# Optimization experiments

Measured on AMD Instinct MI355X. Metric: run time of the kernel, lower is better.

Reference implementation:

```python
import jax, jax.numpy as jnp
import numpy as np

SIGMA = 0.3
EPS = 1e-8  # torch CosineSimilarity eps


def _normal_log_prob(x, sigma=SIGMA):
    # torch.distributions.Normal(1, sigma).log_prob(x)
    return -0.5 * ((x - 1.0) / sigma) ** 2 - jnp.log(sigma) - 0.5 * jnp.log(2.0 * jnp.pi)


def _entropy_term(lp):
    # -(exp(lp) * lp).sum()
    return -jnp.sum(jnp.exp(lp) * lp)


def setup_inputs() -> dict:
    key = jax.random.key(0)
    kx, ky = jax.random.split(key)
    ex = jax.random.normal(kx, (8192, 512), dtype=jnp.float32)
    ey = jax.random.normal(ky, (8192, 512), dtype=jnp.float32)
    return {"ex": ex, "ey": ey}


def reference(ex, ey):
    # cosine similarity matrix C[n, m] = <ex_n, ey_m> / (||ex_n|| * ||ey_m||)
    xn = ex / jnp.maximum(jnp.linalg.norm(ex, axis=-1, keepdims=True), EPS)
    yn = ey / jnp.maximum(jnp.linalg.norm(ey, axis=-1, keepdims=True), EPS)
    C = jnp.einsum('nd,md->nm', xn, yn)  # [N, M]
    # condense_side == 'both'
    lp_right = _normal_log_prob(jnp.max(C, axis=-1))  # [N]
    lp_left = _normal_log_prob(jnp.max(C, axis=0))    # [M]
    return (_entropy_term(lp_right), _entropy_term(lp_left))
```

## Files before the change

### kernel.cpp

```cpp
#include <hip/hip_runtime.h>
#include <hip/hip_bf16.h>
#include <stdint.h>

#define NROWS 8192
#define DIM   512
#define NP    4
#define NSTEP 4
#define NTILE 4
#define FSCALE 16.0f
#define INV_FS2 (1.0f / 256.0f)
#define SCALE1 0x7F7F7F7F

typedef unsigned char u8;
typedef float f32x4 __attribute__((ext_vector_type(4)));
typedef int i32x4 __attribute__((ext_vector_type(4)));
typedef int i32x8 __attribute__((ext_vector_type(8)));

__device__ __forceinline__ unsigned fenc(float f) {
  unsigned u = __float_as_uint(f);
  return (u & 0x80000000u) ? ~u : (u | 0x80000000u);
}
__device__ __forceinline__ float fdec(unsigned u) {
  unsigned b = (u & 0x80000000u) ? (u ^ 0x80000000u) : ~u;
  return __uint_as_float(b);
}

#if __has_builtin(__builtin_amdgcn_cvt_pk_fp8_f32)
#define HAVE_CVT_PK_FP8 1
#else
__device__ __forceinline__ u8 f2e4m3(float f) {
  unsigned u = __float_as_uint(f);
  unsigned sgn = (u >> 24) & 0x80u;
  unsigned au = u & 0x7FFFFFFFu;
  if (au < 0x3C800000u) return (u8)sgn;
  unsigned r = au + 0x7FFFFu + ((au >> 20) & 1u);
  int e = (int)((r >> 23) & 0xFF) - 127;
  unsigned m = (r >> 20) & 7u;
  if (e > 8) return (u8)(sgn | 0x7Eu);
  return (u8)(sgn | ((unsigned)(e + 7) << 3) | m);
}
#endif

__device__ __forceinline__ void async16(const void* g, void* l) {
  __builtin_amdgcn_global_load_lds(
      (const __attribute__((address_space(1))) unsigned int*)g,
      (__attribute__((address_space(3))) unsigned int*)l, 16, 0, 0);
}

__global__ __launch_bounds__(512) void normf_kernel(
    const float* __restrict__ ex, const float* __restrict__ ey,
    u8* __restrict__ Xf, u8* __restrict__ Yf,
    unsigned* __restrict__ enc_init) {
  const int pb = blockIdx.x;
  const int p = pb & 511;
  const float* src = (pb < 512) ? ex : ey;
  u8* dst = (pb < 512) ? Xf : Yf;
  const int t = threadIdx.x, lane = t & 63, w = t >> 6;
  const int fr = lane & 15, hi = lane >> 4;
  if (pb < 32) {
    enc_init[pb * 512 + t] = fenc(-512.0f);
  }
  __shared__ float part[16][8];
  float e[2][8];
  float ss = 0.f;
#pragma unroll
  for (int c = 0; c < 2; ++c) {
    const int q = w + c * 8;
    const float* g = src + (size_t)(p * 16 + fr) * DIM + q * 32 + hi * 8;
    float4 v0 = *(const float4*)g;
    float4 v1 = *(const float4*)(g + 4);
    e[c][0] = v0.x; e[c][1] = v0.y; e[c][2] = v0.z; e[c][3] = v0.w;
    e[c][4] = v1.x; e[c][5] = v1.y; e[c][6] = v1.z; e[c][7] = v1.w;
#pragma unroll
    for (int j = 0; j < 8; ++j) ss += e[c][j] * e[c][j];
  }
  ss += __shfl_xor(ss, 16);
  ss += __shfl_xor(ss, 32);
  if (lane < 16) part[lane][w] = ss;
  __syncthreads();
  float tot = 0.f;
#pragma unroll
  for (int i = 0; i < 8; ++i) tot += part[fr][i];
  const float sc = FSCALE / fmaxf(sqrtf(tot), 1e-8f);
#pragma unroll
  for (int c = 0; c < 2; ++c) {
    const int q = w + c * 8;
#if HAVE_CVT_PK_FP8
    int lo = 0, hi2 = 0;
    lo = __builtin_amdgcn_cvt_pk_fp8_f32(e[c][0] * sc, e[c][1] * sc, lo, false);
    lo = __builtin_amdgcn_cvt_pk_fp8_f32(e[c][2] * sc, e[c][3] * sc, lo, true);
    hi2 = __builtin_amdgcn_cvt_pk_fp8_f32(e[c][4] * sc, e[c][5] * sc, hi2, false);
    hi2 = __builtin_amdgcn_cvt_pk_fp8_f32(e[c][6] * sc, e[c][7] * sc, hi2, true);
    const unsigned long long pk =
        (unsigned long long)(unsigned)lo | ((unsigned long long)(unsigned)hi2 << 32);
#else
    unsigned long long pk = 0;
#pragma unroll
    for (int j = 0; j < 8; ++j)
      pk |= (unsigned long long)f2e4m3(e[c][j] * sc) << (8 * j);
#endif
    const int f = q >> 2;
    const int kg = q & 3;
    const int olane = fr + kg * 16;
    const int half = hi >> 1;
    const size_t addr = (size_t)(p * NP + f) * 2048 + half * 1024 +
                        olane * 16 + (hi & 1) * 8;
    *(unsigned long long*)(dst + addr) = pk;
  }
}

__global__ __launch_bounds__(256, 3) void gemm_max_kernel(
    const u8* __restrict__ Xf, const u8* __restrict__ Yf,
    unsigned* __restrict__ rowmax, unsigned* __restrict__ colmax) {
  __shared__ u8 lds[16][2048];

  const int t = threadIdx.x, lane = t & 63, w = t >> 6;
  const int wr = w >> 1, wc = w & 1;

  const int raw = blockIdx.x, xcd = raw & 7, l = raw >> 3;
  const int brow = (l & 63) * 128;
  const int bcol0 = (xcd * 2 + (l >> 6)) * 512;
  const int browP = brow >> 4;

  f32x4 acc[4][4];
#pragma unroll
  for (int m = 0; m < 4; ++m)
#pragma unroll
    for (int n = 0; n < 4; ++n) acc[m][n] = (f32x4){0.f, 0.f, 0.f, 0.f};

  const u8* gA0 = Xf + (size_t)(browP + 2 * w) * (NP * 2048) + lane * 16;
  const u8* gA1 = Xf + (size_t)(browP + 2 * w + 1) * (NP * 2048) + lane * 16;
  const u8* gBb = Yf + (size_t)(bcol0 >> 4) * (NP * 2048) + lane * 16;

#pragma unroll 1
  for (int u = 0; u < NTILE * NSTEP; ++u) {
    const int h = u & 3;
    const int tileP = (u >> 2) * 8;
    const size_t o = (size_t)h * 2048;
    __syncthreads();
    {
      const u8* gB0 = gBb + (size_t)(tileP + 2 * w) * (NP * 2048);
      const u8* gB1 = gBb + (size_t)(tileP + 2 * w + 1) * (NP * 2048);
#pragma unroll
      for (int half = 0; half < 2; ++half) {
        async16(gA0 + o + half * 1024, &lds[2 * w][half * 1024]);
        async16(gA1 + o + half * 1024, &lds[2 * w + 1][half * 1024]);
        async16(gB0 + o + half * 1024, &lds[8 + 2 * w][half * 1024]);
        async16(gB1 + o + half * 1024, &lds[8 + 2 * w + 1][half * 1024]);
      }
    }
    __syncthreads();
    i32x8 b[4];
#pragma unroll
    for (int n = 0; n < 4; ++n) {
      const u8* base = &lds[8 + wc * 4 + n][0];
      i32x4 lo = *(const i32x4*)(base + lane * 16);
      i32x4 hi = *(const i32x4*)(base + 1024 + lane * 16);
      b[n][0] = lo[0]; b[n][1] = lo[1]; b[n][2] = lo[2]; b[n][3] = lo[3];
      b[n][4] = hi[0]; b[n][5] = hi[1]; b[n][6] = hi[2]; b[n][7] = hi[3];
    }
#pragma unroll
    for (int m = 0; m < 4; ++m) {
      const u8* base = &lds[wr * 4 + m][0];
      i32x4 lo = *(const i32x4*)(base + lane * 16);
      i32x4 hi = *(const i32x4*)(base + 1024 + lane * 16);
      i32x8 a;
      a[0] = lo[0]; a[1] = lo[1]; a[2] = lo[2]; a[3] = lo[3];
      a[4] = hi[0]; a[5] = hi[1]; a[6] = hi[2]; a[7] = hi[3];
#pragma unroll
      for (int n = 0; n < 4; ++n)
        acc[m][n] = __builtin_amdgcn_mfma_scale_f32_16x16x128_f8f6f4(
            a, b[n], acc[m][n], 0, 0, 0, SCALE1, 0, SCALE1);
    }

    if (h == 3) {
      const int bcol = bcol0 + (u >> 2) * 128;
#pragma unroll
      for (int m = 0; m < 4; ++m) {
        f32x4 rm = acc[m][0];
#pragma unroll
        for (int n = 1; n < 4; ++n) {
          rm[0] = fmaxf(rm[0], acc[m][n][0]);
          rm[1] = fmaxf(rm[1], acc[m][n][1]);
          rm[2] = fmaxf(rm[2], acc[m][n][2]);
          rm[3] = fmaxf(rm[3], acc[m][n][3]);
        }
#pragma unroll
        for (int r = 0; r < 4; ++r) {
          float v = rm[r];
          v = fmaxf(v, __shfl_xor(v, 1));
          v = fmaxf(v, __shfl_xor(v, 2));
          v = fmaxf(v, __shfl_xor(v, 4));
          v = fmaxf(v, __shfl_xor(v, 8));
          if ((lane & 15) == 0) {
            const int grow = brow + wr * 64 + m * 16 + (lane >> 4) * 4 + r;
            atomicMax(rowmax + grow, fenc(v));
          }
        }
      }
#pragma unroll
      for (int n = 0; n < 4; ++n) {
        float cm = -512.0f;
#pragma unroll
        for (int m = 0; m < 4; ++m) {
          cm = fmaxf(cm, acc[m][n][0]);
          cm = fmaxf(cm, acc[m][n][1]);
          cm = fmaxf(cm, acc[m][n][2]);
          cm = fmaxf(cm, acc[m][n][3]);
        }
        cm = fmaxf(cm, __shfl_xor(cm, 16));
        cm = fmaxf(cm, __shfl_xor(cm, 32));
        if (lane < 16) {
          const int gcol = bcol + wc * 64 + n * 16 + lane;
          atomicMax(colmax + gcol, fenc(cm));
        }
      }
#pragma unroll
      for (int m = 0; m < 4; ++m)
#pragma unroll
        for (int n = 0; n < 4; ++n) acc[m][n] = (f32x4){0.f, 0.f, 0.f, 0.f};
    }
  }
}

__global__ __launch_bounds__(256) void entropy_kernel(
    const unsigned* __restrict__ enc, float* __restrict__ out) {
  const int which = blockIdx.x;
  const unsigned* e = enc + which * NROWS;
  float s = 0.0f;
  for (int i = threadIdx.x; i < NROWS; i += 256) {
    const float x = fdec(e[i]) * INV_FS2;
    const float z = (x - 1.0f) * (1.0f / 0.3f);
    const float lp = -0.5f * z * z + 0.2850342711439819f;
    s += expf(lp) * lp;
  }
#pragma unroll
  for (int m = 1; m <= 32; m <<= 1) s += __shfl_xor(s, m);
  __shared__ float sr[4];
  if ((threadIdx.x & 63) == 0) sr[threadIdx.x >> 6] = s;
  __syncthreads();
  if (threadIdx.x == 0) out[which] = -(sr[0] + sr[1] + sr[2] + sr[3]);
}

extern "C" void kernel_launch(void* const* d_in, const int* in_sizes, int n_in,
                              void* d_out, int out_size, void* d_ws, size_t ws_size,
                              hipStream_t stream) {
  const float* ex = (const float*)d_in[0];
  const float* ey = (const float*)d_in[1];

  u8* Xf = (u8*)d_ws;
  u8* Yf = Xf + (size_t)NROWS * DIM;
  unsigned* enc = (unsigned*)(Yf + (size_t)NROWS * DIM);
  float* out = (float*)d_out;

  hipLaunchKernelGGL(normf_kernel, dim3(1024), dim3(512), 0, stream,
                     ex, ey, Xf, Yf, enc);
  hipLaunchKernelGGL(gemm_max_kernel, dim3(1024), dim3(256), 0, stream,
                     Xf, Yf, enc, enc + NROWS);
  hipLaunchKernelGGL(entropy_kernel, dim3(2), dim3(256), 0, stream, enc, out);
}
```

Measured before the change: 79.06 us.

## Double-buffer LDS tiles to overlap async global loads with MFMA compute

Doubles the shared memory buffer and prefetches the next K-step's A/B tiles into the alternate buffer while the current step computes. The two barriers per iteration become one, preceded by a vmcnt(0) wait. The aim is to hide global-to-LDS load latency behind the MFMA work. In exchange, LDS use per block rises to 64KB and launch bounds drop from 3 to 2 blocks per CU, which reduces occupancy.

```diff
diff --git a/kernel.cpp b/kernel.cpp
--- a/kernel.cpp
+++ b/kernel.cpp
@@ -7,6 +7,7 @@
 #define NP    4
 #define NSTEP 4
 #define NTILE 4
+#define NU    (NTILE * NSTEP)
 #define FSCALE 16.0f
 #define INV_FS2 (1.0f / 256.0f)
 #define SCALE1 0x7F7F7F7F
@@ -109,10 +110,10 @@
   }
 }
 
-__global__ __launch_bounds__(256, 3) void gemm_max_kernel(
+__global__ __launch_bounds__(256, 2) void gemm_max_kernel(
     const u8* __restrict__ Xf, const u8* __restrict__ Yf,
     unsigned* __restrict__ rowmax, unsigned* __restrict__ colmax) {
-  __shared__ u8 lds[16][2048];
+  __shared__ u8 lds[2][16][2048];
 
   const int t = threadIdx.x, lane = t & 63, w = t >> 6;
   const int wr = w >> 1, wc = w & 1;
@@ -132,28 +133,33 @@
   const u8* gA1 = Xf + (size_t)(browP + 2 * w + 1) * (NP * 2048) + lane * 16;
   const u8* gBb = Yf + (size_t)(bcol0 >> 4) * (NP * 2048) + lane * 16;
 
-#pragma unroll 1
-  for (int u = 0; u < NTILE * NSTEP; ++u) {
+  auto stage = [&](int u, int s) {
     const int h = u & 3;
     const int tileP = (u >> 2) * 8;
     const size_t o = (size_t)h * 2048;
-    __syncthreads();
-    {
-      const u8* gB0 = gBb + (size_t)(tileP + 2 * w) * (NP * 2048);
-      const u8* gB1 = gBb + (size_t)(tileP + 2 * w + 1) * (NP * 2048);
-#pragma unroll
-      for (int half = 0; half < 2; ++half) {
-        async16(gA0 + o + half * 1024, &lds[2 * w][half * 1024]);
-        async16(gA1 + o + half * 1024, &lds[2 * w + 1][half * 1024]);
-        async16(gB0 + o + half * 1024, &lds[8 + 2 * w][half * 1024]);
-        async16(gB1 + o + half * 1024, &lds[8 + 2 * w + 1][half * 1024]);
-      }
-    }
-    __syncthreads();
+    const u8* gB0 = gBb + (size_t)(tileP + 2 * w) * (NP * 2048);
+    const u8* gB1 = gBb + (size_t)(tileP + 2 * w + 1) * (NP * 2048);
+#pragma unroll
+    for (int half = 0; half < 2; ++half) {
+      async16(gA0 + o + half * 1024, &lds[s][2 * w][half * 1024]);
+      async16(gA1 + o + half * 1024, &lds[s][2 * w + 1][half * 1024]);
+      async16(gB0 + o + half * 1024, &lds[s][8 + 2 * w][half * 1024]);
+      async16(gB1 + o + half * 1024, &lds[s][8 + 2 * w + 1][half * 1024]);
+    }
+  };
+
+  stage(0, 0);
+
+#pragma unroll 1
+  for (int u = 0; u < NU; ++u) {
+    asm volatile("s_waitcnt vmcnt(0)" ::: "memory");
+    __builtin_amdgcn_s_barrier();
+    if (u < NU - 1) stage(u + 1, (u + 1) & 1);
+    const int s = u & 1;
     i32x8 b[4];
 #pragma unroll
     for (int n = 0; n < 4; ++n) {
-      const u8* base = &lds[8 + wc * 4 + n][0];
+      const u8* base = &lds[s][8 + wc * 4 + n][0];
       i32x4 lo = *(const i32x4*)(base + lane * 16);
       i32x4 hi = *(const i32x4*)(base + 1024 + lane * 16);
       b[n][0] = lo[0]; b[n][1] = lo[1]; b[n][2] = lo[2]; b[n][3] = lo[3];
@@ -161,7 +167,7 @@
     }
 #pragma unroll
     for (int m = 0; m < 4; ++m) {
-      const u8* base = &lds[wr * 4 + m][0];
+      const u8* base = &lds[s][wr * 4 + m][0];
       i32x4 lo = *(const i32x4*)(base + lane * 16);
       i32x4 hi = *(const i32x4*)(base + 1024 + lane * 16);
       i32x8 a;
@@ -173,7 +179,7 @@
             a, b[n], acc[m][n], 0, 0, 0, SCALE1, 0, SCALE1);
     }
 
-    if (h == 3) {
+    if ((u & 3) == 3) {
       const int bcol = bcol0 + (u >> 2) * 128;
 #pragma unroll
       for (int m = 0; m < 4; ++m) {
```

Measured after the change: 86.93 us. 10.0% more time.
